# Optimization experiments

Measured on AMD Instinct MI355X. Metric: run time of the kernel, lower is better.

## Reference

```python
import jax, jax.numpy as jnp
import numpy as np

N = 4096   # nodes per side
B = 32     # graphs per batch
E = 65536  # edges per side
D = 128    # hidden dim
L = 4      # layers
H = 4      # heads


def setup_inputs() -> dict:
    key = jax.random.key(0)
    ks = jax.random.split(key, 20)
    s = 1.0 / np.sqrt(D)
    inp = {
        'x_s': jax.random.normal(ks[0], (N, D), jnp.float32),
        'x_t': jax.random.normal(ks[1], (N, D), jnp.float32),
        'edge_index_s': jax.random.randint(ks[2], (2, E), 0, N),
        'edge_attr_s': jax.random.uniform(ks[3], (E, D), jnp.float32),
        'edge_index_t': jax.random.randint(ks[4], (2, E), 0, N),
        'edge_attr_t': jax.random.uniform(ks[5], (E, D), jnp.float32),
        'batch_s': jnp.repeat(jnp.arange(B), N // B),
        'batch_t': jnp.repeat(jnp.arange(B), N // B),
        # stacked per-layer parameters (torch Linear layout: [out, in])
        'gnn_rel_w': jax.random.normal(ks[6], (L, D, D), jnp.float32) * s,
        'gnn_rel_b': jnp.zeros((L, D), jnp.float32),
        'gnn_root_w': jax.random.normal(ks[7], (L, D, D), jnp.float32) * s,
        'attn_in_w': jax.random.normal(ks[8], (L, 3 * D, D), jnp.float32) * s,
        'attn_in_b': jnp.zeros((L, 3 * D), jnp.float32),
        'attn_out_w': jax.random.normal(ks[9], (L, D, D), jnp.float32) * s,
        'attn_out_b': jnp.zeros((L, D), jnp.float32),
        'ln_g': jnp.ones((L, D), jnp.float32),
        'ln_b': jnp.zeros((L, D), jnp.float32),
        'gate_w': jax.random.normal(ks[10], (D, 1), jnp.float32) * s,
        'gate_b': jnp.zeros((1,), jnp.float32),
    }
    return inp


def _graph_conv(x, src, dst, ew, w_rel, b_rel, w_root):
    # message = edge_weight * x_j, aggr='mean' over target nodes
    msg = ew * x[src]                                   # [E, D]
    agg = jax.ops.segment_sum(msg, dst, num_segments=N)
    cnt = jax.ops.segment_sum(jnp.ones((msg.shape[0], 1), x.dtype), dst, num_segments=N)
    mean = agg / jnp.maximum(cnt, 1.0)
    return mean @ w_rel.T + b_rel + x @ w_root.T


def _mha(qx, kx, w_in, b_in, w_out, b_out, mask):
    dh = D // H
    q = (qx @ w_in[:D].T + b_in[:D]).reshape(-1, H, dh)
    k = (kx @ w_in[D:2 * D].T + b_in[D:2 * D]).reshape(-1, H, dh)
    v = (kx @ w_in[2 * D:].T + b_in[2 * D:]).reshape(-1, H, dh)
    scores = jnp.einsum('qhd,khd->hqk', q, k) * (1.0 / np.sqrt(dh))
    scores = jnp.where(mask[None], -jnp.inf, scores)
    a = jax.nn.softmax(scores, axis=-1)
    o = jnp.einsum('hqk,khd->qhd', a, v).reshape(-1, D)
    return o @ w_out.T + b_out


def _layernorm(x, g, b, eps=1e-5):
    mu = jnp.mean(x, axis=-1, keepdims=True)
    var = jnp.mean((x - mu) ** 2, axis=-1, keepdims=True)
    return (x - mu) * jax.lax.rsqrt(var + eps) * g + b


def _pool(x, batch, gw, gb):
    # GlobalAttention: gate = sigmoid(Linear(x)); softmax per graph; weighted sum
    gate = jax.nn.sigmoid(x @ gw + gb)                  # [N, 1]
    m = jax.ops.segment_max(gate, batch, num_segments=B)
    e = jnp.exp(gate - m[batch])
    z = jax.ops.segment_sum(e, batch, num_segments=B)
    alpha = e / z[batch]
    return jax.ops.segment_sum(alpha * x, batch, num_segments=B)  # [B, D]


def reference(x_s, x_t, edge_index_s, edge_attr_s, edge_index_t, edge_attr_t,
              batch_s, batch_t, gnn_rel_w, gnn_rel_b, gnn_root_w,
              attn_in_w, attn_in_b, attn_out_w, attn_out_b, ln_g, ln_b,
              gate_w, gate_b):
    src_s, dst_s = edge_index_s[0], edge_index_s[1]
    src_t, dst_t = edge_index_t[0], edge_index_t[1]
    mask = batch_s[:, None] != batch_t[None, :]         # True = blocked
    for i in range(L):
        x_s = _graph_conv(x_s, src_s, dst_s, edge_attr_s, gnn_rel_w[i], gnn_rel_b[i], gnn_root_w[i])
        x_t = _graph_conv(x_t, src_t, dst_t, edge_attr_t, gnn_rel_w[i], gnn_rel_b[i], gnn_root_w[i])
        o_s = _mha(x_s, x_t, attn_in_w[i], attn_in_b[i], attn_out_w[i], attn_out_b[i], mask)
        o_t = _mha(x_t, x_s, attn_in_w[i], attn_in_b[i], attn_out_w[i], attn_out_b[i], mask.T)
        x_s = _layernorm(o_s, ln_g[i], ln_b[i])
        x_t = _layernorm(o_t, ln_g[i], ln_b[i])
    p_s = _pool(x_s, batch_s, gate_w, gate_b)
    p_t = _pool(x_t, batch_t, gate_w, gate_b)
    p_s = p_s / jnp.maximum(jnp.linalg.norm(p_s, axis=-1, keepdims=True), 1e-12)
    p_t = p_t / jnp.maximum(jnp.linalg.norm(p_t, axis=-1, keepdims=True), 1e-12)
    return jnp.sum(p_s * p_t, axis=-1)                  # [B]
```

## Files before the change

kernel.cpp:

```cpp
#include <hip/hip_runtime.h>
#include <math.h>

#define N_NODES 4096
#define NROWS   8192
#define BGRAPH  32
#define NEDGE   65536
#define DIM     128
#define NLAYER  4
#define NHEAD   4
#define DHEAD   32
#define QDIM    384

typedef _Float16 half8v __attribute__((ext_vector_type(8)));
typedef _Float16 half4v __attribute__((ext_vector_type(4)));
typedef _Float16 half2v __attribute__((ext_vector_type(2)));
typedef float f32x4 __attribute__((ext_vector_type(4)));

__device__ inline f32x4 MFMA(half8v a, half8v b, f32x4 c) {
    return __builtin_amdgcn_mfma_f32_16x16x32_f16(a, b, c, 0, 0, 0);
}

__device__ inline void cvt4(const float* __restrict__ s, _Float16* __restrict__ d, int i) {
    float4 v = ((const float4*)s)[i];
    half4v h;
    h[0] = (_Float16)v.x; h[1] = (_Float16)v.y;
    h[2] = (_Float16)v.z; h[3] = (_Float16)v.w;
    *(half4v*)(d + (size_t)i * 4) = h;
}

__global__ __launch_bounds__(256) void cvt16_kernel(
    const float* __restrict__ x_s, const float* __restrict__ x_t,
    const float* __restrict__ out_w, const float* __restrict__ in_w,
    const float* __restrict__ root_w, const float* __restrict__ rel_w,
    const int* __restrict__ dst_s, const int* __restrict__ dst_t,
    _Float16* __restrict__ x16, _Float16* __restrict__ outw16,
    _Float16* __restrict__ in16, _Float16* __restrict__ bt16,
    int* __restrict__ cnt)
{
    int gid = blockIdx.x * 256 + threadIdx.x, gs = gridDim.x * 256;
    const int nx = N_NODES * DIM / 4;
    const int nw = NLAYER * DIM * DIM / 4;
    const int ni = NLAYER * QDIM * DIM / 4;
    for (int i = gid; i < nx; i += gs) cvt4(x_s, x16, i);
    for (int i = gid; i < nx; i += gs) cvt4(x_t, x16 + N_NODES * DIM, i);
    for (int i = gid; i < nw; i += gs) cvt4(out_w, outw16, i);
    for (int i = gid; i < ni; i += gs) cvt4(in_w, in16, i);
    const int nb = NLAYER * 2 * DIM * DIM;
    for (int i = gid; i < nb; i += gs) {
        int j = i & 127, k = (i >> 7) & 127, m = (i >> 14) & 1, L = i >> 15;
        const float* B = (m ? rel_w : root_w) + (size_t)L * DIM * DIM;
        bt16[i] = (_Float16)B[j * DIM + k];
    }
    for (int i = gid; i < 2 * NEDGE; i += gs) {
        int side = i >> 16, e = i & (NEDGE - 1);
        const int* dd = side ? dst_t : dst_s;
        atomicAdd(&cnt[side * N_NODES + dd[e]], 1);
    }
}

__global__ __launch_bounds__(256) void scan_kernel(
    const int* __restrict__ cnt, int* __restrict__ row_start, int* __restrict__ cursor)
{
    int side = blockIdx.x;
    int t = threadIdx.x;
    __shared__ int part[256];
    int local[16];
    int s = 0;
    #pragma unroll
    for (int j = 0; j < 16; ++j) { local[j] = cnt[side * N_NODES + t * 16 + j]; s += local[j]; }
    part[t] = s;
    __syncthreads();
    for (int off = 1; off < 256; off <<= 1) {
        int v = (t >= off) ? part[t - off] : 0;
        __syncthreads();
        part[t] += v;
        __syncthreads();
    }
    int run = (t == 0) ? 0 : part[t - 1];
    #pragma unroll
    for (int j = 0; j < 16; ++j) {
        int idx = t * 16 + j;
        row_start[side * (N_NODES + 1) + idx] = run;
        cursor[side * N_NODES + idx] = run;
        run += local[j];
    }
    if (t == 255) row_start[side * (N_NODES + 1) + N_NODES] = run;
}

__global__ __launch_bounds__(256) void rg_kernel(
    const int* __restrict__ src_s, const int* __restrict__ dst_s,
    const int* __restrict__ src_t, const int* __restrict__ dst_t,
    const float* __restrict__ ea_s, const float* __restrict__ ea_t,
    int* __restrict__ cursor, int* __restrict__ srcs, _Float16* __restrict__ ea16s)
{
    int t = threadIdx.x;
    int g16 = t >> 4, sub = t & 15, lane = t & 63;
    int ef = blockIdx.x * 16 + g16;
    int side = ef >> 16, e = ef & (NEDGE - 1);
    const int* dd = side ? dst_t : dst_s;
    const int* ss = side ? src_t : src_s;
    const float* ea = side ? ea_t : ea_s;
    int pos = 0;
    if (sub == 0) pos = atomicAdd(&cursor[side * N_NODES + dd[e]], 1);
    pos = __shfl(pos, lane & ~15);
    if (sub == 0) srcs[side * NEDGE + pos] = ss[e];
    const float* sp = ea + (size_t)e * DIM + sub * 8;
    float4 v0 = *(const float4*)(sp);
    float4 v1 = *(const float4*)(sp + 4);
    half8v h;
    h[0]=(_Float16)v0.x; h[1]=(_Float16)v0.y; h[2]=(_Float16)v0.z; h[3]=(_Float16)v0.w;
    h[4]=(_Float16)v1.x; h[5]=(_Float16)v1.y; h[6]=(_Float16)v1.z; h[7]=(_Float16)v1.w;
    *(half8v*)(ea16s + (size_t)(side * NEDGE + pos) * DIM + sub * 8) = h;
}

__global__ __launch_bounds__(256) void wfold_mfma(
    const _Float16* __restrict__ in16, const _Float16* __restrict__ bt16,
    _Float16* __restrict__ wq16)
{
    int lm = blockIdx.z;
    const _Float16* A = in16 + (size_t)(lm >> 1) * QDIM * DIM;
    const _Float16* B = bt16 + (size_t)lm * DIM * DIM;
    _Float16* C = wq16 + (size_t)lm * QDIM * DIM;
    int tid = threadIdx.x;
    int wave = tid >> 6, lane = tid & 63;
    int wm = wave >> 1, wn = wave & 1;
    int row0 = blockIdx.x * 64 + wm * 32;
    int col0 = blockIdx.y * 64 + wn * 32;
    int lr = lane & 15;
    int lk = (lane >> 4) * 8;
    f32x4 zero = {0.f, 0.f, 0.f, 0.f};
    f32x4 acc[2][2] = {{zero, zero}, {zero, zero}};
    const _Float16* Ap0 = A + (size_t)(row0 + lr) * DIM + lk;
    const _Float16* Ap1 = A + (size_t)(row0 + 16 + lr) * DIM + lk;
    const _Float16* Bp0 = B + (size_t)(col0 + lr) * DIM + lk;
    const _Float16* Bp1 = B + (size_t)(col0 + 16 + lr) * DIM + lk;
    #pragma unroll
    for (int k0 = 0; k0 < DIM; k0 += 32) {
        half8v a0 = *(const half8v*)(Ap0 + k0);
        half8v a1 = *(const half8v*)(Ap1 + k0);
        half8v b0 = *(const half8v*)(Bp0 + k0);
        half8v b1 = *(const half8v*)(Bp1 + k0);
        acc[0][0] = MFMA(a0, b0, acc[0][0]);
        acc[0][1] = MFMA(a0, b1, acc[0][1]);
        acc[1][0] = MFMA(a1, b0, acc[1][0]);
        acc[1][1] = MFMA(a1, b1, acc[1][1]);
    }
    int g4 = (lane >> 4) * 4;
    #pragma unroll
    for (int fc = 0; fc < 2; ++fc) {
        int col = col0 + fc * 16 + lr;
        #pragma unroll
        for (int fr = 0; fr < 2; ++fr) {
            int rbase = row0 + fr * 16 + g4;
            #pragma unroll
            for (int j = 0; j < 4; ++j)
                C[(size_t)(rbase + j) * DIM + col] = (_Float16)acc[fr][fc][j];
        }
    }
}

__global__ __launch_bounds__(256) void beff_kernel(
    const float* __restrict__ in_w, const float* __restrict__ in_b,
    const float* __restrict__ rel_b, float* __restrict__ beff)
{
    int gid = blockIdx.x * 256 + threadIdx.x;
    if (gid >= NLAYER * QDIM) return;
    int L = gid / QDIM, i = gid % QDIM;
    const float* Win = in_w + (size_t)L * QDIM * DIM;
    const float* br = rel_b + (size_t)L * DIM;
    float s = in_b[(size_t)L * QDIM + i];
    #pragma unroll 4
    for (int j = 0; j < DIM; ++j) s += Win[(size_t)i * DIM + j] * br[j];
    beff[gid] = s;
}

__global__ __launch_bounds__(64) void agg_kernel(
    const int* __restrict__ srcs, const _Float16* __restrict__ ea16s,
    const int* __restrict__ row_start,
    const _Float16* __restrict__ x16, _Float16* __restrict__ agg16)
{
    int n = blockIdx.x, side = blockIdx.y;
    int lane = threadIdx.x;
    const int* sp = srcs + side * NEDGE;
    const _Float16* ep = ea16s + (size_t)side * NEDGE * DIM + lane * 2;
    const _Float16* xp = x16 + (size_t)side * N_NODES * DIM + lane * 2;
    int rs = row_start[side * (N_NODES + 1) + n];
    int re = row_start[side * (N_NODES + 1) + n + 1];
    float ax = 0.f, ay = 0.f;
    int i = rs;
    for (; i + 2 <= re; i += 2) {
        int s0 = sp[i], s1 = sp[i + 1];
        half2v w0 = *(const half2v*)(ep + (size_t)i * DIM);
        half2v w1 = *(const half2v*)(ep + (size_t)(i + 1) * DIM);
        half2v x0 = *(const half2v*)(xp + (size_t)s0 * DIM);
        half2v x1 = *(const half2v*)(xp + (size_t)s1 * DIM);
        ax += (float)w0[0] * (float)x0[0] + (float)w1[0] * (float)x1[0];
        ay += (float)w0[1] * (float)x0[1] + (float)w1[1] * (float)x1[1];
    }
    if (i < re) {
        int s0 = sp[i];
        half2v w0 = *(const half2v*)(ep + (size_t)i * DIM);
        half2v x0 = *(const half2v*)(xp + (size_t)s0 * DIM);
        ax += (float)w0[0] * (float)x0[0];
        ay += (float)w0[1] * (float)x0[1];
    }
    float sc = 1.0f / (float)max(re - rs, 1);
    half2v o; o[0] = (_Float16)(ax * sc); o[1] = (_Float16)(ay * sc);
    *(half2v*)(agg16 + (size_t)(side * N_NODES + n) * DIM + lane * 2) = o;
}

__global__ __launch_bounds__(256) void qkv2_mfma(
    const _Float16* __restrict__ x16, const _Float16* __restrict__ agg16,
    const _Float16* __restrict__ wq,
    const float* __restrict__ beff,
    _Float16* __restrict__ qb16)
{
    int tid = threadIdx.x;
    int wave = tid >> 6, lane = tid & 63;
    int wm = wave >> 1, wn = wave & 1;
    int row0 = blockIdx.x * 64 + wm * 32;
    int col0 = blockIdx.y * 64 + wn * 32;
    int lr = lane & 15;
    int lk = (lane >> 4) * 8;
    f32x4 zero = {0.f, 0.f, 0.f, 0.f};
    f32x4 acc[2][2] = {{zero, zero}, {zero, zero}};
    #pragma unroll
    for (int s = 0; s < 2; ++s) {
        const _Float16* A = s ? agg16 : x16;
        const _Float16* W = wq + (size_t)s * QDIM * DIM;
        const _Float16* Ap0 = A + (size_t)(row0 + lr) * DIM + lk;
        const _Float16* Ap1 = A + (size_t)(row0 + 16 + lr) * DIM + lk;
        const _Float16* Wp0 = W + (size_t)(col0 + lr) * DIM + lk;
        const _Float16* Wp1 = W + (size_t)(col0 + 16 + lr) * DIM + lk;
        #pragma unroll
        for (int k0 = 0; k0 < DIM; k0 += 32) {
            half8v a0 = *(const half8v*)(Ap0 + k0);
            half8v a1 = *(const half8v*)(Ap1 + k0);
            half8v b0 = *(const half8v*)(Wp0 + k0);
            half8v b1 = *(const half8v*)(Wp1 + k0);
            acc[0][0] = MFMA(a0, b0, acc[0][0]);
            acc[0][1] = MFMA(a0, b1, acc[0][1]);
            acc[1][0] = MFMA(a1, b0, acc[1][0]);
            acc[1][1] = MFMA(a1, b1, acc[1][1]);
        }
    }
    int g4 = (lane >> 4) * 4;
    #pragma unroll
    for (int fc = 0; fc < 2; ++fc) {
        int col = col0 + fc * 16 + lr;
        float bv = beff[col];
        #pragma unroll
        for (int fr = 0; fr < 2; ++fr) {
            int rbase = row0 + fr * 16 + g4;
            #pragma unroll
            for (int j = 0; j < 4; ++j) {
                float v = acc[fr][fc][j] + bv;
                qb16[(size_t)(rbase + j) * QDIM + col] = (_Float16)v;
            }
        }
    }
}

__global__ __launch_bounds__(256) void attn_oln_kernel(
    const _Float16* __restrict__ qkv, const _Float16* __restrict__ outw,
    const float* __restrict__ bias, const float* __restrict__ gamma,
    const float* __restrict__ beta, _Float16* __restrict__ x16out)
{
    int g = blockIdx.x, dir = blockIdx.y, rb = blockIdx.z;
    int qoff  = dir ? N_NODES : 0;
    int kvoff = dir ? 0 : N_NODES;
    int t = threadIdx.x;
    int w = t >> 6, lane = t & 63;
    int lr = lane & 15, g4 = lane >> 4;
    __shared__ _Float16 VT[NHEAD][32][136];
    __shared__ _Float16 P[NHEAD][16][136];
    __shared__ float red_s[16][5], red_q[16][5];
    f32x4 zero = {0.f, 0.f, 0.f, 0.f};
    for (int kk = lane; kk < 128; kk += 64) {
        const _Float16* vp = qkv + (size_t)(kvoff + g * 128 + kk) * QDIM + 2 * DIM + w * DHEAD;
        half8v v0 = *(const half8v*)(vp);
        half8v v1 = *(const half8v*)(vp + 8);
        half8v v2 = *(const half8v*)(vp + 16);
        half8v v3 = *(const half8v*)(vp + 24);
        #pragma unroll
        for (int j = 0; j < 8; ++j) {
            VT[w][j][kk]      = v0[j];
            VT[w][8 + j][kk]  = v1[j];
            VT[w][16 + j][kk] = v2[j];
            VT[w][24 + j][kk] = v3[j];
        }
    }
    int qrow0 = qoff + g * 128 + rb * 16;
    const _Float16* qp = qkv + (size_t)(qrow0 + lr) * QDIM + w * DHEAD + g4 * 8;
    half8v qfrag = *(const half8v*)qp;
    f32x4 S[8];
    #pragma unroll
    for (int kf = 0; kf < 8; ++kf) {
        const _Float16* kp = qkv + (size_t)(kvoff + g * 128 + kf * 16 + lr) * QDIM
                             + DIM + w * DHEAD + g4 * 8;
        S[kf] = MFMA(qfrag, *(const half8v*)kp, zero);
    }
    const float scale = 0.17677669529663687f;
    #pragma unroll
    for (int j = 0; j < 4; ++j) {
        float m = -INFINITY;
        #pragma unroll
        for (int kf = 0; kf < 8; ++kf) m = fmaxf(m, S[kf][j]);
        m *= scale;
        #pragma unroll
        for (int mk = 1; mk < 16; mk <<= 1) m = fmaxf(m, __shfl_xor(m, mk));
        float pj[8];
        float l = 0.f;
        #pragma unroll
        for (int kf = 0; kf < 8; ++kf) {
            float pv = __expf(S[kf][j] * scale - m);
            pj[kf] = pv; l += pv;
        }
        #pragma unroll
        for (int mk = 1; mk < 16; mk <<= 1) l += __shfl_xor(l, mk);
        float linv = 1.0f / l;
        int row = g4 * 4 + j;
        #pragma unroll
        for (int kf = 0; kf < 8; ++kf)
            P[w][row][kf * 16 + lr] = (_Float16)(pj[kf] * linv);
    }
    f32x4 O[2] = {zero, zero};
    #pragma unroll
    for (int ks = 0; ks < 4; ++ks) {
        half8v pa = *(const half8v*)&P[w][lr][ks * 32 + g4 * 8];
        #pragma unroll
        for (int df = 0; df < 2; ++df) {
            half8v vb = *(const half8v*)&VT[w][df * 16 + lr][ks * 32 + g4 * 8];
            O[df] = MFMA(pa, vb, O[df]);
        }
    }
    __syncthreads();
    _Float16 (*OL)[136] = P[0];
    #pragma unroll
    for (int df = 0; df < 2; ++df)
        #pragma unroll
        for (int j = 0; j < 4; ++j)
            OL[g4 * 4 + j][w * DHEAD + df * 16 + lr] = (_Float16)O[df][j];
    __syncthreads();
    f32x4 acc2[2] = {zero, zero};
    #pragma unroll
    for (int kk = 0; kk < 4; ++kk) {
        half8v a = *(const half8v*)&OL[lr][kk * 32 + g4 * 8];
        #pragma unroll
        for (int ct = 0; ct < 2; ++ct) {
            const _Float16* wp = outw + (size_t)(w * 32 + ct * 16 + lr) * DIM + kk * 32 + g4 * 8;
            acc2[ct] = MFMA(a, *(const half8v*)wp, acc2[ct]);
        }
    }
    float v[2][4];
    #pragma unroll
    for (int ct = 0; ct < 2; ++ct) {
        float bv = bias[w * 32 + ct * 16 + lr];
        #pragma unroll
        for (int j = 0; j < 4; ++j) v[ct][j] = acc2[ct][j] + bv;
    }
    #pragma unroll
    for (int j = 0; j < 4; ++j) {
        float ss = v[0][j] + v[1][j];
        float qq = v[0][j] * v[0][j] + v[1][j] * v[1][j];
        #pragma unroll
        for (int mk = 1; mk < 16; mk <<= 1) {
            ss += __shfl_xor(ss, mk);
            qq += __shfl_xor(qq, mk);
        }
        if (lr == 0) {
            red_s[g4 * 4 + j][w] = ss;
            red_q[g4 * 4 + j][w] = qq;
        }
    }
    __syncthreads();
    #pragma unroll
    for (int j = 0; j < 4; ++j) {
        int row = g4 * 4 + j;
        float Sv = red_s[row][0] + red_s[row][1] + red_s[row][2] + red_s[row][3];
        float Qv = red_q[row][0] + red_q[row][1] + red_q[row][2] + red_q[row][3];
        float mu = Sv * (1.0f / 128.0f);
        float inv = rsqrtf(Qv * (1.0f / 128.0f) - mu * mu + 1e-5f);
        #pragma unroll
        for (int ct = 0; ct < 2; ++ct) {
            int col = w * 32 + ct * 16 + lr;
            float o = (v[ct][j] - mu) * inv * gamma[col] + beta[col];
            x16out[(size_t)(qrow0 + row) * DIM + col] = (_Float16)o;
        }
    }
}

__global__ __launch_bounds__(256) void poolcos_kernel(
    const _Float16* __restrict__ x16, const float* __restrict__ gw,
    const float* __restrict__ gb, float* __restrict__ out)
{
    int g = blockIdx.x, t = threadIdx.x;
    int side = t >> 7, r = t & 127;
    __shared__ float sm[2][128];
    __shared__ float al[2][128];
    __shared__ float pl[2][DIM];
    const _Float16* xr = x16 + (size_t)(side * N_NODES + g * 128 + r) * DIM;
    float dot = gb[0];
    #pragma unroll
    for (int d = 0; d < DIM; d += 8) {
        half8v xv = *(const half8v*)(xr + d);
        #pragma unroll
        for (int u = 0; u < 8; ++u) dot += (float)xv[u] * gw[d + u];
    }
    float gate = 1.0f / (1.0f + __expf(-dot));
    sm[side][r] = gate; __syncthreads();
    for (int sN = 64; sN > 0; sN >>= 1) {
        if (r < sN) sm[side][r] = fmaxf(sm[side][r], sm[side][r + sN]);
        __syncthreads();
    }
    float m = sm[side][0]; __syncthreads();
    float e = __expf(gate - m);
    sm[side][r] = e; __syncthreads();
    for (int sN = 64; sN > 0; sN >>= 1) {
        if (r < sN) sm[side][r] += sm[side][r + sN];
        __syncthreads();
    }
    al[side][r] = e / sm[side][0];
    __syncthreads();
    int d = t & 127;
    float acc = 0.0f;
    const _Float16* xg = x16 + (size_t)(side * N_NODES + g * 128) * DIM;
    for (int n = 0; n < 128; ++n) acc += al[side][n] * (float)xg[(size_t)n * DIM + d];
    pl[side][d] = acc;
    __syncthreads();
    if (t < 64) {
        float a0 = pl[0][t], a1 = pl[0][64 + t];
        float b0 = pl[1][t], b1 = pl[1][64 + t];
        float saa = a0 * a0 + a1 * a1;
        float sbb = b0 * b0 + b1 * b1;
        float sab = a0 * b0 + a1 * b1;
        #pragma unroll
        for (int off = 32; off; off >>= 1) {
            saa += __shfl_down(saa, off);
            sbb += __shfl_down(sbb, off);
            sab += __shfl_down(sab, off);
        }
        if (t == 0) {
            float na = fmaxf(sqrtf(saa), 1e-12f);
            float nb = fmaxf(sqrtf(sbb), 1e-12f);
            out[g] = sab / (na * nb);
        }
    }
}

extern "C" void kernel_launch(void* const* d_in, const int* in_sizes, int n_in,
                              void* d_out, int out_size, void* d_ws, size_t ws_size,
                              hipStream_t stream)
{
    const float* x_s    = (const float*)d_in[0];
    const float* x_t    = (const float*)d_in[1];
    const int*   ei_s   = (const int*)d_in[2];
    const float* ea_s   = (const float*)d_in[3];
    const int*   ei_t   = (const int*)d_in[4];
    const float* ea_t   = (const float*)d_in[5];
    const float* rel_w  = (const float*)d_in[8];
    const float* rel_b  = (const float*)d_in[9];
    const float* root_w = (const float*)d_in[10];
    const float* in_w   = (const float*)d_in[11];
    const float* in_b   = (const float*)d_in[12];
    const float* out_w  = (const float*)d_in[13];
    const float* out_b  = (const float*)d_in[14];
    const float* g_ln   = (const float*)d_in[15];
    const float* b_ln   = (const float*)d_in[16];
    const float* gate_w = (const float*)d_in[17];
    const float* gate_b = (const float*)d_in[18];
    float* out = (float*)d_out;

    const size_t RD = (size_t)NROWS * DIM;
    _Float16* h16p = (_Float16*)d_ws;
    _Float16* x16    = h16p; h16p += RD;
    _Float16* agg16  = h16p; h16p += RD;
    _Float16* qb16   = h16p; h16p += RD * 3;
    _Float16* ea16s  = h16p; h16p += (size_t)2 * NEDGE * DIM;
    _Float16* outw16 = h16p; h16p += (size_t)NLAYER * DIM * DIM;
    _Float16* wq16   = h16p; h16p += (size_t)NLAYER * 2 * QDIM * DIM;
    _Float16* in16   = h16p; h16p += (size_t)NLAYER * QDIM * DIM;
    _Float16* bt16   = h16p; h16p += (size_t)NLAYER * 2 * DIM * DIM;
    float* fws = (float*)h16p;
    float* beff = fws; fws += NLAYER * QDIM;
    int* iws = (int*)fws;
    int* cnt       = iws; iws += 2 * N_NODES;
    int* cursor    = iws; iws += 2 * N_NODES;
    int* row_start = iws; iws += 2 * (N_NODES + 1);
    int* srcs      = iws; iws += 2 * NEDGE;

    const int* src_s = ei_s, *dst_s = ei_s + NEDGE;
    const int* src_t = ei_t, *dst_t = ei_t + NEDGE;

    hipMemsetAsync(cnt, 0, 2 * N_NODES * 4, stream);
    cvt16_kernel<<<512, 256, 0, stream>>>(x_s, x_t, out_w, in_w, root_w, rel_w,
                                          dst_s, dst_t, x16, outw16, in16, bt16, cnt);
    scan_kernel<<<2, 256, 0, stream>>>(cnt, row_start, cursor);
    rg_kernel<<<2 * NEDGE / 16, 256, 0, stream>>>(src_s, dst_s, src_t, dst_t,
                                                  ea_s, ea_t, cursor, srcs, ea16s);
    {
        dim3 gw(QDIM / 64, DIM / 64, NLAYER * 2);
        wfold_mfma<<<gw, 256, 0, stream>>>(in16, bt16, wq16);
    }
    beff_kernel<<<(NLAYER * QDIM + 255) / 256, 256, 0, stream>>>(in_w, in_b, rel_b, beff);

    dim3 gq(NROWS / 64, QDIM / 64);
    dim3 gagg(N_NODES, 2);
    dim3 gattn(BGRAPH, 2, 8);

    for (int i = 0; i < NLAYER; ++i) {
        const _Float16* wq   = wq16   + (size_t)i * 2 * QDIM * DIM;
        const float*    be   = beff   + (size_t)i * QDIM;
        const _Float16* wout = outw16 + (size_t)i * DIM * DIM;
        const float*    bout = out_b  + (size_t)i * DIM;
        const float*    lg   = g_ln   + (size_t)i * DIM;
        const float*    lb   = b_ln   + (size_t)i * DIM;

        agg_kernel<<<gagg, 64, 0, stream>>>(srcs, ea16s, row_start, x16, agg16);
        qkv2_mfma<<<gq, 256, 0, stream>>>(x16, agg16, wq, be, qb16);
        attn_oln_kernel<<<gattn, 256, 0, stream>>>(qb16, wout, bout, lg, lb, x16);
    }

    poolcos_kernel<<<BGRAPH, 256, 0, stream>>>(x16, gate_w, gate_b, out);
}
```

Before: 207.0 us.

## Merge setup kernels, split agg edges across half-waves, unroll pool reduction

Three independent changes. The scan, weight-fold MFMA and bias-fold kernels are merged into one launch, with the block index selecting the role, which removes two launches from the setup chain. The aggregation kernel now has each half-wave handle alternate edges using 4-wide fp16 loads, then combines the two halves with a cross-lane shuffle, aiming for more memory parallelism per node. The pooling loop uses four independent accumulators to shorten the dependency chain; this changes the fp32 summation order slightly.

```diff
diff --git a/kernel.cpp b/kernel.cpp
--- a/kernel.cpp
+++ b/kernel.cpp
@@ -58,33 +58,93 @@
     }
 }
 
-__global__ __launch_bounds__(256) void scan_kernel(
-    const int* __restrict__ cnt, int* __restrict__ row_start, int* __restrict__ cursor)
-{
-    int side = blockIdx.x;
+__global__ __launch_bounds__(256) void setup2_kernel(
+    const int* __restrict__ cnt, int* __restrict__ row_start, int* __restrict__ cursor,
+    const _Float16* __restrict__ in16, const _Float16* __restrict__ bt16,
+    _Float16* __restrict__ wq16,
+    const float* __restrict__ in_w, const float* __restrict__ in_b,
+    const float* __restrict__ rel_b, float* __restrict__ beff)
+{
+    int b = blockIdx.x;
     int t = threadIdx.x;
-    __shared__ int part[256];
-    int local[16];
-    int s = 0;
-    #pragma unroll
-    for (int j = 0; j < 16; ++j) { local[j] = cnt[side * N_NODES + t * 16 + j]; s += local[j]; }
-    part[t] = s;
-    __syncthreads();
-    for (int off = 1; off < 256; off <<= 1) {
-        int v = (t >= off) ? part[t - off] : 0;
+    if (b < 2) {
+        int side = b;
+        __shared__ int part[256];
+        int local[16];
+        int s = 0;
+        #pragma unroll
+        for (int j = 0; j < 16; ++j) { local[j] = cnt[side * N_NODES + t * 16 + j]; s += local[j]; }
+        part[t] = s;
         __syncthreads();
-        part[t] += v;
-        __syncthreads();
-    }
-    int run = (t == 0) ? 0 : part[t - 1];
-    #pragma unroll
-    for (int j = 0; j < 16; ++j) {
-        int idx = t * 16 + j;
-        row_start[side * (N_NODES + 1) + idx] = run;
-        cursor[side * N_NODES + idx] = run;
-        run += local[j];
-    }
-    if (t == 255) row_start[side * (N_NODES + 1) + N_NODES] = run;
+        for (int off = 1; off < 256; off <<= 1) {
+            int v = (t >= off) ? part[t - off] : 0;
+            __syncthreads();
+            part[t] += v;
+            __syncthreads();
+        }
+        int run = (t == 0) ? 0 : part[t - 1];
+        #pragma unroll
+        for (int j = 0; j < 16; ++j) {
+            int idx = t * 16 + j;
+            row_start[side * (N_NODES + 1) + idx] = run;
+            cursor[side * N_NODES + idx] = run;
+            run += local[j];
+        }
+        if (t == 255) row_start[side * (N_NODES + 1) + N_NODES] = run;
+    } else if (b < 98) {
+        int b2 = b - 2;
+        int bx = b2 % 6;
+        int by = (b2 / 6) % 2;
+        int lm = b2 / 12;
+        const _Float16* A = in16 + (size_t)(lm >> 1) * QDIM * DIM;
+        const _Float16* B = bt16 + (size_t)lm * DIM * DIM;
+        _Float16* C = wq16 + (size_t)lm * QDIM * DIM;
+        int wave = t >> 6, lane = t & 63;
+        int wm = wave >> 1, wn = wave & 1;
+        int row0 = bx * 64 + wm * 32;
+        int col0 = by * 64 + wn * 32;
+        int lr = lane & 15;
+        int lk = (lane >> 4) * 8;
+        f32x4 zero = {0.f, 0.f, 0.f, 0.f};
+        f32x4 acc[2][2] = {{zero, zero}, {zero, zero}};
+        const _Float16* Ap0 = A + (size_t)(row0 + lr) * DIM + lk;
+        const _Float16* Ap1 = A + (size_t)(row0 + 16 + lr) * DIM + lk;
+        const _Float16* Bp0 = B + (size_t)(col0 + lr) * DIM + lk;
+        const _Float16* Bp1 = B + (size_t)(col0 + 16 + lr) * DIM + lk;
+        #pragma unroll
+        for (int k0 = 0; k0 < DIM; k0 += 32) {
+            half8v a0 = *(const half8v*)(Ap0 + k0);
+            half8v a1 = *(const half8v*)(Ap1 + k0);
+            half8v b0 = *(const half8v*)(Bp0 + k0);
+            half8v b1 = *(const half8v*)(Bp1 + k0);
+            acc[0][0] = MFMA(a0, b0, acc[0][0]);
+            acc[0][1] = MFMA(a0, b1, acc[0][1]);
+            acc[1][0] = MFMA(a1, b0, acc[1][0]);
+            acc[1][1] = MFMA(a1, b1, acc[1][1]);
+        }
+        int g4 = (lane >> 4) * 4;
+        #pragma unroll
+        for (int fc = 0; fc < 2; ++fc) {
+            int col = col0 + fc * 16 + lr;
+            #pragma unroll
+            for (int fr = 0; fr < 2; ++fr) {
+                int rbase = row0 + fr * 16 + g4;
+                #pragma unroll
+                for (int j = 0; j < 4; ++j)
+                    C[(size_t)(rbase + j) * DIM + col] = (_Float16)acc[fr][fc][j];
+            }
+        }
+    } else {
+        int gid = (b - 98) * 256 + t;
+        if (gid >= NLAYER * QDIM) return;
+        int L = gid / QDIM, i = gid % QDIM;
+        const float* Win = in_w + (size_t)L * QDIM * DIM;
+        const float* br = rel_b + (size_t)L * DIM;
+        float s = in_b[(size_t)L * QDIM + i];
+        #pragma unroll 4
+        for (int j = 0; j < DIM; ++j) s += Win[(size_t)i * DIM + j] * br[j];
+        beff[gid] = s;
+    }
 }
 
 __global__ __launch_bounds__(256) void rg_kernel(
@@ -113,67 +173,6 @@
     *(half8v*)(ea16s + (size_t)(side * NEDGE + pos) * DIM + sub * 8) = h;
 }
 
-__global__ __launch_bounds__(256) void wfold_mfma(
-    const _Float16* __restrict__ in16, const _Float16* __restrict__ bt16,
-    _Float16* __restrict__ wq16)
-{
-    int lm = blockIdx.z;
-    const _Float16* A = in16 + (size_t)(lm >> 1) * QDIM * DIM;
-    const _Float16* B = bt16 + (size_t)lm * DIM * DIM;
-    _Float16* C = wq16 + (size_t)lm * QDIM * DIM;
-    int tid = threadIdx.x;
-    int wave = tid >> 6, lane = tid & 63;
-    int wm = wave >> 1, wn = wave & 1;
-    int row0 = blockIdx.x * 64 + wm * 32;
-    int col0 = blockIdx.y * 64 + wn * 32;
-    int lr = lane & 15;
-    int lk = (lane >> 4) * 8;
-    f32x4 zero = {0.f, 0.f, 0.f, 0.f};
-    f32x4 acc[2][2] = {{zero, zero}, {zero, zero}};
-    const _Float16* Ap0 = A + (size_t)(row0 + lr) * DIM + lk;
-    const _Float16* Ap1 = A + (size_t)(row0 + 16 + lr) * DIM + lk;
-    const _Float16* Bp0 = B + (size_t)(col0 + lr) * DIM + lk;
-    const _Float16* Bp1 = B + (size_t)(col0 + 16 + lr) * DIM + lk;
-    #pragma unroll
-    for (int k0 = 0; k0 < DIM; k0 += 32) {
-        half8v a0 = *(const half8v*)(Ap0 + k0);
-        half8v a1 = *(const half8v*)(Ap1 + k0);
-        half8v b0 = *(const half8v*)(Bp0 + k0);
-        half8v b1 = *(const half8v*)(Bp1 + k0);
-        acc[0][0] = MFMA(a0, b0, acc[0][0]);
-        acc[0][1] = MFMA(a0, b1, acc[0][1]);
-        acc[1][0] = MFMA(a1, b0, acc[1][0]);
-        acc[1][1] = MFMA(a1, b1, acc[1][1]);
-    }
-    int g4 = (lane >> 4) * 4;
-    #pragma unroll
-    for (int fc = 0; fc < 2; ++fc) {
-        int col = col0 + fc * 16 + lr;
-        #pragma unroll
-        for (int fr = 0; fr < 2; ++fr) {
-            int rbase = row0 + fr * 16 + g4;
-            #pragma unroll
-            for (int j = 0; j < 4; ++j)
-                C[(size_t)(rbase + j) * DIM + col] = (_Float16)acc[fr][fc][j];
-        }
-    }
-}
-
-__global__ __launch_bounds__(256) void beff_kernel(
-    const float* __restrict__ in_w, const float* __restrict__ in_b,
-    const float* __restrict__ rel_b, float* __restrict__ beff)
-{
-    int gid = blockIdx.x * 256 + threadIdx.x;
-    if (gid >= NLAYER * QDIM) return;
-    int L = gid / QDIM, i = gid % QDIM;
-    const float* Win = in_w + (size_t)L * QDIM * DIM;
-    const float* br = rel_b + (size_t)L * DIM;
-    float s = in_b[(size_t)L * QDIM + i];
-    #pragma unroll 4
-    for (int j = 0; j < DIM; ++j) s += Win[(size_t)i * DIM + j] * br[j];
-    beff[gid] = s;
-}
-
 __global__ __launch_bounds__(64) void agg_kernel(
     const int* __restrict__ srcs, const _Float16* __restrict__ ea16s,
     const int* __restrict__ row_start,
@@ -181,32 +180,34 @@
 {
     int n = blockIdx.x, side = blockIdx.y;
     int lane = threadIdx.x;
+    int half = lane >> 5;
+    int sub = lane & 31;
     const int* sp = srcs + side * NEDGE;
-    const _Float16* ep = ea16s + (size_t)side * NEDGE * DIM + lane * 2;
-    const _Float16* xp = x16 + (size_t)side * N_NODES * DIM + lane * 2;
+    const _Float16* ep = ea16s + (size_t)side * NEDGE * DIM + sub * 4;
+    const _Float16* xp = x16 + (size_t)side * N_NODES * DIM + sub * 4;
     int rs = row_start[side * (N_NODES + 1) + n];
     int re = row_start[side * (N_NODES + 1) + n + 1];
-    float ax = 0.f, ay = 0.f;
-    int i = rs;
-    for (; i + 2 <= re; i += 2) {
-        int s0 = sp[i], s1 = sp[i + 1];
-        half2v w0 = *(const half2v*)(ep + (size_t)i * DIM);
-        half2v w1 = *(const half2v*)(ep + (size_t)(i + 1) * DIM);
-        half2v x0 = *(const half2v*)(xp + (size_t)s0 * DIM);
-        half2v x1 = *(const half2v*)(xp + (size_t)s1 * DIM);
-        ax += (float)w0[0] * (float)x0[0] + (float)w1[0] * (float)x1[0];
-        ay += (float)w0[1] * (float)x0[1] + (float)w1[1] * (float)x1[1];
-    }
-    if (i < re) {
-        int s0 = sp[i];
-        half2v w0 = *(const half2v*)(ep + (size_t)i * DIM);
-        half2v x0 = *(const half2v*)(xp + (size_t)s0 * DIM);
-        ax += (float)w0[0] * (float)x0[0];
-        ay += (float)w0[1] * (float)x0[1];
-    }
-    float sc = 1.0f / (float)max(re - rs, 1);
-    half2v o; o[0] = (_Float16)(ax * sc); o[1] = (_Float16)(ay * sc);
-    *(half2v*)(agg16 + (size_t)(side * N_NODES + n) * DIM + lane * 2) = o;
+    float a0 = 0.f, a1 = 0.f, a2 = 0.f, a3 = 0.f;
+    for (int i = rs + half; i < re; i += 2) {
+        int s = sp[i];
+        half4v w = *(const half4v*)(ep + (size_t)i * DIM);
+        half4v xv = *(const half4v*)(xp + (size_t)s * DIM);
+        a0 += (float)w[0] * (float)xv[0];
+        a1 += (float)w[1] * (float)xv[1];
+        a2 += (float)w[2] * (float)xv[2];
+        a3 += (float)w[3] * (float)xv[3];
+    }
+    a0 += __shfl_xor(a0, 32);
+    a1 += __shfl_xor(a1, 32);
+    a2 += __shfl_xor(a2, 32);
+    a3 += __shfl_xor(a3, 32);
+    if (half == 0) {
+        float sc = 1.0f / (float)max(re - rs, 1);
+        half4v o;
+        o[0] = (_Float16)(a0 * sc); o[1] = (_Float16)(a1 * sc);
+        o[2] = (_Float16)(a2 * sc); o[3] = (_Float16)(a3 * sc);
+        *(half4v*)(agg16 + (size_t)(side * N_NODES + n) * DIM + sub * 4) = o;
+    }
 }
 
 __global__ __launch_bounds__(256) void qkv2_mfma(
@@ -423,10 +424,16 @@
     al[side][r] = e / sm[side][0];
     __syncthreads();
     int d = t & 127;
-    float acc = 0.0f;
+    float acc0 = 0.0f, acc1 = 0.0f, acc2 = 0.0f, acc3 = 0.0f;
     const _Float16* xg = x16 + (size_t)(side * N_NODES + g * 128) * DIM;
-    for (int n = 0; n < 128; ++n) acc += al[side][n] * (float)xg[(size_t)n * DIM + d];
-    pl[side][d] = acc;
+    #pragma unroll 4
+    for (int n = 0; n < 128; n += 4) {
+        acc0 += al[side][n]     * (float)xg[(size_t)n * DIM + d];
+        acc1 += al[side][n + 1] * (float)xg[(size_t)(n + 1) * DIM + d];
+        acc2 += al[side][n + 2] * (float)xg[(size_t)(n + 2) * DIM + d];
+        acc3 += al[side][n + 3] * (float)xg[(size_t)(n + 3) * DIM + d];
+    }
+    pl[side][d] = (acc0 + acc1) + (acc2 + acc3);
     __syncthreads();
     if (t < 64) {
         float a0 = pl[0][t], a1 = pl[0][64 + t];
@@ -495,14 +502,10 @@
     hipMemsetAsync(cnt, 0, 2 * N_NODES * 4, stream);
     cvt16_kernel<<<512, 256, 0, stream>>>(x_s, x_t, out_w, in_w, root_w, rel_w,
                                           dst_s, dst_t, x16, outw16, in16, bt16, cnt);
-    scan_kernel<<<2, 256, 0, stream>>>(cnt, row_start, cursor);
+    setup2_kernel<<<104, 256, 0, stream>>>(cnt, row_start, cursor, in16, bt16, wq16,
+                                           in_w, in_b, rel_b, beff);
     rg_kernel<<<2 * NEDGE / 16, 256, 0, stream>>>(src_s, dst_s, src_t, dst_t,
                                                   ea_s, ea_t, cursor, srcs, ea16s);
-    {
-        dim3 gw(QDIM / 64, DIM / 64, NLAYER * 2);
-        wfold_mfma<<<gw, 256, 0, stream>>>(in16, bt16, wq16);
-    }
-    beff_kernel<<<(NLAYER * QDIM + 255) / 256, 256, 0, stream>>>(in_w, in_b, rel_b, beff);
 
     dim3 gq(NROWS / 64, QDIM / 64);
     dim3 gagg(N_NODES, 2);
```

Result: no change. 205.3 us (-0.8%).
